# Optimization experiments

Hardware: AMD Instinct MI355X
Metric: run time of the kernel (lower is better)

## Reference

```python
import jax, jax.numpy as jnp
import numpy as np

HEAD_DIM = 64
NUM_HEADS = 16
ROPE_BASE = 10000.0


def _rope_cos_sin(seq_len, head_dim, dtype):
    inv_freq = 1.0 / (ROPE_BASE ** (jnp.arange(0, head_dim, 2, dtype=jnp.float32) / head_dim))
    t = jnp.arange(seq_len, dtype=jnp.float32)
    freqs = jnp.outer(t, inv_freq)                      # [S, D/2]
    emb = jnp.concatenate([freqs, freqs], axis=-1)      # [S, D]
    return jnp.cos(emb).astype(dtype), jnp.sin(emb).astype(dtype)


def _rotate_half(x):
    x1, x2 = jnp.split(x, 2, axis=-1)
    return jnp.concatenate([-x2, x1], axis=-1)


def setup_inputs() -> dict:
    key = jax.random.key(0)
    ks = jax.random.split(key, 5)
    B, S, H = 2, 2048, 1024
    x = jax.random.normal(ks[0], (B, S, H), dtype=jnp.float32)
    attention_mask = jnp.ones((B, S), dtype=jnp.float32)
    scale = 0.02
    Wq = jax.random.normal(ks[1], (H, H), dtype=jnp.float32) * scale
    Wk = jax.random.normal(ks[2], (H, H), dtype=jnp.float32) * scale
    Wv = jax.random.normal(ks[3], (H, H), dtype=jnp.float32) * scale
    Wo = jax.random.normal(ks[4], (H, H), dtype=jnp.float32) * scale
    return {"x": x, "attention_mask": attention_mask, "Wq": Wq, "Wk": Wk, "Wv": Wv, "Wo": Wo}


def reference(x, attention_mask, Wq, Wk, Wv, Wo):
    B, S, H = x.shape
    nh, hd = NUM_HEADS, HEAD_DIM
    scale = hd ** -0.5

    # nn.Linear semantics: y = x @ W^T  (W is [out, in])
    q = jnp.einsum('bsh,oh->bso', x, Wq).reshape(B, S, nh, hd).transpose(0, 2, 1, 3)
    k = jnp.einsum('bsh,oh->bso', x, Wk).reshape(B, S, nh, hd).transpose(0, 2, 1, 3)
    v = jnp.einsum('bsh,oh->bso', x, Wv).reshape(B, S, nh, hd).transpose(0, 2, 1, 3)

    cos, sin = _rope_cos_sin(S, hd, x.dtype)            # [S, hd]
    cos = cos[None, None, :, :]
    sin = sin[None, None, :, :]
    q = q * cos + _rotate_half(q) * sin
    k = k * cos + _rotate_half(k) * sin

    attn = jnp.einsum('bhqd,bhkd->bhqk', q, k) * scale  # [B, nh, S, S]
    mask = (1.0 - attention_mask.astype(x.dtype))[:, None, None, :] * jnp.finfo(x.dtype).min
    attn = attn + mask
    attn = jax.nn.softmax(attn, axis=-1)
    out = jnp.einsum('bhqk,bhkd->bhqd', attn, v)        # [B, nh, S, hd]
    out = out.transpose(0, 2, 1, 3).reshape(B, S, nh * hd)
    return jnp.einsum('bso,ho->bsh', out, Wo)
```

## Files before the change

kernel.cpp:

```cpp
#include <hip/hip_runtime.h>
#include <math.h>

#define BB 2
#define SS 2048
#define HH 1024
#define NH 16
#define HD 64
#define MM (BB*SS)

typedef __attribute__((ext_vector_type(8))) _Float16 f16x8;
typedef __attribute__((ext_vector_type(2))) __fp16 hf16x2;
typedef __attribute__((ext_vector_type(4))) float f32x4;
typedef __attribute__((ext_vector_type(16))) float f32x16;

#define QSCALE 0.18033688011112042f

__device__ __forceinline__ unsigned short f2h(float f) {
    union { _Float16 h; unsigned short u; } c;
    c.h = (_Float16)f;
    return c.u;
}

__device__ __forceinline__ unsigned int pkh(float a, float b) {
    union { hf16x2 h; unsigned int u; } c;
    c.h = __builtin_amdgcn_cvt_pkrtz(a, b);
    return c.u;
}

__device__ __forceinline__ void gld16(const void* g, void* s) {
    __builtin_amdgcn_global_load_lds(
        (const __attribute__((address_space(1))) void*)g,
        (__attribute__((address_space(3))) void*)s, 16, 0, 0);
}

__global__ __launch_bounds__(256) void prep(
    const float* __restrict__ x, const float* __restrict__ mask,
    const float* __restrict__ Wq, const float* __restrict__ Wk,
    const float* __restrict__ Wv, const float* __restrict__ Wo,
    unsigned short* __restrict__ xf, unsigned short* __restrict__ wf,
    float* __restrict__ ctab, float* __restrict__ stab, float* __restrict__ mt,
    unsigned int* __restrict__ mflag)
{
    int gtid = blockIdx.x * 256 + threadIdx.x;
    if (gtid < SS * 32) {
        int s = gtid >> 5, i = gtid & 31;
        double invf = pow(10000.0, -(double)i / 32.0);
        double a = (double)s * invf;
        ctab[gtid] = (float)cos(a);
        stab[gtid] = (float)sin(a);
    }
    if (gtid < BB * SS) {
        float mv = mask[gtid];
        mt[gtid] = (1.0f - mv) * (-1.0e38f);
        unsigned long long bal = __ballot(mv == 1.0f);
        if ((threadIdx.x & 63) == 0)
            mflag[gtid >> 6] = (bal == ~0ull) ? 1u : 0u;
    }
    for (int it = gtid; it < 2097152; it += 524288) {
        float4 v; unsigned short* d; size_t off;
        if (it < 1048576) {
            off = (size_t)it * 4;
            v = *(const float4*)(x + off);
            d = xf;
        } else {
            off = (size_t)(it - 1048576) * 4;
            int row = (int)(off >> 10);
            const float* W = row < 1024 ? Wq : row < 2048 ? Wk : row < 3072 ? Wv : Wo;
            v = *(const float4*)(W + (((size_t)(row & 1023)) << 10) + (off & 1023));
            d = wf;
        }
        *(ushort4*)(d + off) = make_ushort4(f2h(v.x), f2h(v.y), f2h(v.z), f2h(v.w));
    }
}

template<int MODE>
__global__ __launch_bounds__(256, 3) void gemm3(
    const unsigned short* __restrict__ Axf,
    const unsigned short* __restrict__ Wf,
    const float* __restrict__ ctab, const float* __restrict__ stab,
    unsigned short* __restrict__ qo, unsigned short* __restrict__ ko,
    unsigned short* __restrict__ vo, float* __restrict__ fout)
{
    __shared__ __align__(16) short lsA[2][128*32];
    __shared__ __align__(16) short lsB[2][128*32];

    const int t = threadIdx.x;
    const int m0 = blockIdx.x * 128;
    const int brow0 = (MODE == 0 ? 0 : 3072) + blockIdx.y * 128;
    const int lane = t & 63, wv = t >> 6;
    const int wm = (wv >> 1) * 64, wn = (wv & 1) * 64;
    const int fr = lane & 15, fg = lane >> 4;

    const int srow = t >> 2, pc = t & 3;
    const int scx = (pc ^ ((srow >> 1) & 3)) * 8;
    const int lo  = srow * 32 + pc * 8;
    const size_t gA0 = (size_t)(m0 + srow) * HH + scx;
    const size_t gA1 = (size_t)(m0 + 64 + srow) * HH + scx;
    const size_t gB0 = (size_t)(brow0 + srow) * HH + scx;
    const size_t gB1 = (size_t)(brow0 + 64 + srow) * HH + scx;

    f32x4 acc[4][4] = {};

#define STAGE(sel, kk) do { \
        gld16(Axf + gA0 + (kk), &lsA[sel][lo]);            \
        gld16(Wf  + gB0 + (kk), &lsB[sel][lo]);            \
        gld16(Axf + gA1 + (kk), &lsA[sel][lo + 64*32]);    \
        gld16(Wf  + gB1 + (kk), &lsB[sel][lo + 64*32]);    \
    } while (0)

    STAGE(0, 0);
    __syncthreads();

    int cur = 0;
    for (int k0 = 0; k0 < HH; k0 += 32) {
        if (k0 + 32 < HH) STAGE(cur ^ 1, k0 + 32);

        f16x8 ah[4], bh[4];
        const int swz = (fg ^ ((fr >> 1) & 3)) * 8;
        #pragma unroll
        for (int mi = 0; mi < 4; ++mi)
            ah[mi] = *(const f16x8*)&lsA[cur][(wm + 16*mi + fr)*32 + swz];
        #pragma unroll
        for (int ni = 0; ni < 4; ++ni)
            bh[ni] = *(const f16x8*)&lsB[cur][(wn + 16*ni + fr)*32 + swz];

        __builtin_amdgcn_s_setprio(1);
        #pragma unroll
        for (int mi = 0; mi < 4; ++mi)
            #pragma unroll
            for (int ni = 0; ni < 4; ++ni)
                acc[mi][ni] = __builtin_amdgcn_mfma_f32_16x16x32_f16(ah[mi], bh[ni], acc[mi][ni], 0, 0, 0);
        __builtin_amdgcn_s_setprio(0);
        __syncthreads();
        cur ^= 1;
    }
#undef STAGE

    if (MODE == 0) {
        const int mat = brow0 >> 10;
        const int obase = (brow0 & 1023) + wn;
        const int h = obase >> 6;
        #pragma unroll
        for (int mi = 0; mi < 4; ++mi)
            #pragma unroll
            for (int rr = 0; rr < 4; ++rr) {
                int m = m0 + wm + 16*mi + 4*fg + rr;
                int b = m >> 11, s = m & (SS - 1);
                float v[4];
                #pragma unroll
                for (int ni = 0; ni < 4; ++ni) v[ni] = acc[mi][ni][rr];
                if (mat < 2) {
                    #pragma unroll
                    for (int ni = 0; ni < 2; ++ni) {
                        int i = 16*ni + fr;
                        float c = ctab[s*32 + i], sn = stab[s*32 + i];
                        float v1 = v[ni], v2 = v[ni + 2];
                        v[ni]     = v1*c - v2*sn;
                        v[ni + 2] = v2*c + v1*sn;
                    }
                }
                if (mat == 0) {
                    #pragma unroll
                    for (int ni = 0; ni < 4; ++ni) v[ni] *= QSCALE;
                }
                size_t base = ((size_t)(b*NH + h) * SS + s) * HD;
                #pragma unroll
                for (int ni = 0; ni < 4; ++ni) {
                    int d = 16*ni + fr;
                    unsigned short hb = f2h(v[ni]);
                    if (mat == 0)      qo[base + d] = hb;
                    else if (mat == 1) ko[base + (d ^ ((s & 7) << 3))] = hb;
                    else {
                        size_t va = ((size_t)(b*NH + h) * HD + d) * SS
                                  + (s & ~63) + ((s & 63) ^ ((d & 7) << 3));
                        vo[va] = hb;
                    }
                }
            }
    } else {
        const int n0 = blockIdx.y * 128 + wn;
        #pragma unroll
        for (int mi = 0; mi < 4; ++mi)
            #pragma unroll
            for (int rr = 0; rr < 4; ++rr) {
                int m = m0 + wm + 16*mi + 4*fg + rr;
                #pragma unroll
                for (int ni = 0; ni < 4; ++ni)
                    fout[(size_t)m * HH + n0 + 16*ni + fr] = acc[mi][ni][rr];
            }
    }
}

__global__ __launch_bounds__(256, 2) void attn(
    const unsigned short* __restrict__ qg, const unsigned short* __restrict__ kg,
    const unsigned short* __restrict__ vtg, const float* __restrict__ mt,
    const unsigned int* __restrict__ mfl, unsigned short* __restrict__ cf)
{
    __shared__ __align__(16) short Ks[2][64*64];
    __shared__ __align__(16) short Vs[2][64*64];

    const int t = threadIdx.x, lane = t & 63, wv = t >> 6;
    const int ql = lane & 31;
    const int u  = lane >> 5;
    const int qx = ql & 7;
    const int flat = blockIdx.x;
    const int bh = (flat & 7) + ((flat >> 7) << 3);
    const int q0 = ((flat >> 3) & 15) * 128;
    const int b = bh >> 4, h = bh & 15;

    const unsigned short* kgb = kg  + (size_t)bh*SS*HD;
    const unsigned short* vgb = vtg + (size_t)bh*HD*SS;
    const float* mtb = mt + (size_t)b*SS;
    const unsigned int* mfb = mfl + b*32;

    f16x8 qa[4];
    #pragma unroll
    for (int dc = 0; dc < 4; ++dc)
        qa[dc] = *(const f16x8*)&qg[((size_t)bh*SS + q0 + 32*wv + ql)*HD + 16*dc + 8*u];

    f32x16 o[2] = {};
    float lpart = 0.f;

    const int srow = t >> 3, sg = t & 7;

    gld16(kgb + (size_t)srow*HD + sg*8,      &Ks[0][srow*64 + sg*8]);
    gld16(kgb + (size_t)(32+srow)*HD + sg*8, &Ks[0][(32+srow)*64 + sg*8]);
    gld16(vgb + (size_t)srow*SS + sg*8,      &Vs[0][srow*64 + sg*8]);
    gld16(vgb + (size_t)(32+srow)*SS + sg*8, &Vs[0][(32+srow)*64 + sg*8]);
    __syncthreads();

    int cur = 0;
    for (int kt = 0; kt < SS/64; ++kt) {
        const int k0 = kt * 64;
        if (kt + 1 < SS/64) {
            const int kn = k0 + 64;
            gld16(kgb + (size_t)(kn+srow)*HD + sg*8,      &Ks[cur^1][srow*64 + sg*8]);
            gld16(kgb + (size_t)(kn+32+srow)*HD + sg*8,   &Ks[cur^1][(32+srow)*64 + sg*8]);
            gld16(vgb + (size_t)srow*SS + kn + sg*8,      &Vs[cur^1][srow*64 + sg*8]);
            gld16(vgb + (size_t)(32+srow)*SS + kn + sg*8, &Vs[cur^1][(32+srow)*64 + sg*8]);
        }
        const int fl = __builtin_amdgcn_readfirstlane(mfb[kt]);

        f16x8 kb[2][4];
        #pragma unroll
        for (int ktl = 0; ktl < 2; ++ktl)
            #pragma unroll
            for (int dc = 0; dc < 4; ++dc)
                kb[ktl][dc] = *(const f16x8*)&Ks[cur][(32*ktl + ql)*64 + ((2*dc + u) ^ qx)*8];

        f32x16 sc[2] = {};
        __builtin_amdgcn_s_setprio(1);
        #pragma unroll
        for (int dc = 0; dc < 4; ++dc)
            #pragma unroll
            for (int ktl = 0; ktl < 2; ++ktl)
                sc[ktl] = __builtin_amdgcn_mfma_f32_32x32x16_f16(kb[ktl][dc], qa[dc], sc[ktl], 0, 0, 0);
        __builtin_amdgcn_s_setprio(0);

        f16x8 vb[2][4];
        #pragma unroll
        for (int dt = 0; dt < 2; ++dt)
            #pragma unroll
            for (int ki = 0; ki < 4; ++ki)
                vb[dt][ki] = *(const f16x8*)&Vs[cur][(32*dt + ql)*64 + ((2*ki + u) ^ qx)*8];

        if (fl) {
            #pragma unroll
            for (int ktl = 0; ktl < 2; ++ktl)
                #pragma unroll
                for (int r = 0; r < 16; ++r) {
                    float p = __builtin_amdgcn_exp2f(sc[ktl][r]);
                    sc[ktl][r] = p;
                    lpart += p;
                }
        } else {
            #pragma unroll
            for (int ktl = 0; ktl < 2; ++ktl)
                #pragma unroll
                for (int g = 0; g < 4; ++g) {
                    float4 m4 = *(const float4*)&mtb[k0 + 32*ktl + 8*g + 4*u];
                    #pragma unroll
                    for (int j = 0; j < 4; ++j) {
                        float p = __builtin_amdgcn_exp2f(sc[ktl][4*g + j] + (&m4.x)[j]);
                        sc[ktl][4*g + j] = p;
                        lpart += p;
                    }
                }
        }

        __builtin_amdgcn_s_setprio(1);
        #pragma unroll
        for (int ki = 0; ki < 4; ++ki) {
            const int ktl = ki >> 1;
            const int R0 = 8 * (ki & 1);
            unsigned int A0 = pkh(sc[ktl][R0+0], sc[ktl][R0+1]);
            unsigned int A1 = pkh(sc[ktl][R0+2], sc[ktl][R0+3]);
            unsigned int B0 = pkh(sc[ktl][R0+4], sc[ktl][R0+5]);
            unsigned int B1 = pkh(sc[ktl][R0+6], sc[ktl][R0+7]);
            asm volatile("v_permlane32_swap_b32 %0, %1" : "+v"(A0), "+v"(B0));
            asm volatile("v_permlane32_swap_b32 %0, %1" : "+v"(A1), "+v"(B1));
            union { unsigned int w[4]; f16x8 v; } pf;
            pf.w[0] = A0; pf.w[1] = A1; pf.w[2] = B0; pf.w[3] = B1;
            #pragma unroll
            for (int dt = 0; dt < 2; ++dt)
                o[dt] = __builtin_amdgcn_mfma_f32_32x32x16_f16(vb[dt][ki], pf.v, o[dt], 0, 0, 0);
        }
        __builtin_amdgcn_s_setprio(0);
        __syncthreads();
        cur ^= 1;
    }

    float l = lpart + __shfl_xor(lpart, 32);
    float inv = 1.0f / l;
    size_t base = ((size_t)b*SS + q0 + 32*wv + ql)*HH + h*HD;
    #pragma unroll
    for (int dt = 0; dt < 2; ++dt)
        #pragma unroll
        for (int g = 0; g < 4; ++g) {
            uint2 w;
            w.x = pkh(o[dt][4*g+0]*inv, o[dt][4*g+1]*inv);
            w.y = pkh(o[dt][4*g+2]*inv, o[dt][4*g+3]*inv);
            *(uint2*)&cf[base + 32*dt + 8*g + 4*u] = w;
        }
}

extern "C" void kernel_launch(void* const* d_in, const int* in_sizes, int n_in,
                              void* d_out, int out_size, void* d_ws, size_t ws_size,
                              hipStream_t stream) {
    const float* x    = (const float*)d_in[0];
    const float* mask = (const float*)d_in[1];
    const float* Wq   = (const float*)d_in[2];
    const float* Wk   = (const float*)d_in[3];
    const float* Wv   = (const float*)d_in[4];
    const float* Wo   = (const float*)d_in[5];
    float* out = (float*)d_out;

    const size_t T = (size_t)MM * HH;
    unsigned short* xf = (unsigned short*)d_ws;
    unsigned short* wf = xf + T;
    unsigned short* qt = wf + T;
    unsigned short* kt = qt + T;
    unsigned short* vt = kt + T;
    float* ctab = (float*)(vt + T);
    float* stab = ctab + SS*32;
    float* mt   = stab + SS*32;
    unsigned int* mfg = (unsigned int*)(mt + BB*SS);
    unsigned short* cf = xf;

    prep<<<2048, 256, 0, stream>>>(x, mask, Wq, Wk, Wv, Wo, xf, wf, ctab, stab, mt, mfg);
    gemm3<0><<<dim3(MM/128, 3*HH/128), 256, 0, stream>>>(xf, wf, ctab, stab,
                                                         qt, kt, vt, nullptr);
    attn<<<512, 256, 0, stream>>>(qt, kt, vt, mt, mfg, cf);
    gemm3<1><<<dim3(MM/128, HH/128), 256, 0, stream>>>(cf, wf, nullptr, nullptr,
                                                       nullptr, nullptr, nullptr, out);
}
```

Baseline: 114.5 us.

## Split attention key tiles across waves and reduce partial outputs through LDS

Each attention block now covers 64 queries instead of 128, and its four waves form a 2x2 split: two query halves times two key halves of every 64-key tile. The grid doubles to 1024 blocks, and launch bounds go from 2 to 4 blocks per CU to fit the smaller per-wave register state. At the end, the partial row sums and output accumulators from the second key-half waves are combined through shared memory. This trades more K/V tile loads per query and an extra LDS reduction with barriers for higher occupancy and more blocks to spread across the GPU.

```diff
diff --git a/kernel.cpp b/kernel.cpp
--- a/kernel.cpp
+++ b/kernel.cpp
@@ -191,7 +191,7 @@
     }
 }
 
-__global__ __launch_bounds__(256, 2) void attn(
+__global__ __launch_bounds__(256, 4) void attn(
     const unsigned short* __restrict__ qg, const unsigned short* __restrict__ kg,
     const unsigned short* __restrict__ vtg, const float* __restrict__ mt,
     const unsigned int* __restrict__ mfl, unsigned short* __restrict__ cf)
@@ -203,9 +203,10 @@
     const int ql = lane & 31;
     const int u  = lane >> 5;
     const int qx = ql & 7;
+    const int qh = wv & 1, kh = wv >> 1;
     const int flat = blockIdx.x;
-    const int bh = (flat & 7) + ((flat >> 7) << 3);
-    const int q0 = ((flat >> 3) & 15) * 128;
+    const int bh = (flat & 7) + ((flat >> 8) << 3);
+    const int q0 = ((flat >> 3) & 31) * 64;
     const int b = bh >> 4, h = bh & 15;
 
     const unsigned short* kgb = kg  + (size_t)bh*SS*HD;
@@ -216,7 +217,7 @@
     f16x8 qa[4];
     #pragma unroll
     for (int dc = 0; dc < 4; ++dc)
-        qa[dc] = *(const f16x8*)&qg[((size_t)bh*SS + q0 + 32*wv + ql)*HD + 16*dc + 8*u];
+        qa[dc] = *(const f16x8*)&qg[((size_t)bh*SS + q0 + 32*qh + ql)*HD + 16*dc + 8*u];
 
     f32x16 o[2] = {};
     float lpart = 0.f;
@@ -241,62 +242,53 @@
         }
         const int fl = __builtin_amdgcn_readfirstlane(mfb[kt]);
 
-        f16x8 kb[2][4];
-        #pragma unroll
-        for (int ktl = 0; ktl < 2; ++ktl)
-            #pragma unroll
-            for (int dc = 0; dc < 4; ++dc)
-                kb[ktl][dc] = *(const f16x8*)&Ks[cur][(32*ktl + ql)*64 + ((2*dc + u) ^ qx)*8];
-
-        f32x16 sc[2] = {};
+        f16x8 kb[4];
+        #pragma unroll
+        for (int dc = 0; dc < 4; ++dc)
+            kb[dc] = *(const f16x8*)&Ks[cur][(32*kh + ql)*64 + ((2*dc + u) ^ qx)*8];
+
+        f32x16 sc = {};
         __builtin_amdgcn_s_setprio(1);
         #pragma unroll
         for (int dc = 0; dc < 4; ++dc)
-            #pragma unroll
-            for (int ktl = 0; ktl < 2; ++ktl)
-                sc[ktl] = __builtin_amdgcn_mfma_f32_32x32x16_f16(kb[ktl][dc], qa[dc], sc[ktl], 0, 0, 0);
+            sc = __builtin_amdgcn_mfma_f32_32x32x16_f16(kb[dc], qa[dc], sc, 0, 0, 0);
         __builtin_amdgcn_s_setprio(0);
 
-        f16x8 vb[2][4];
+        f16x8 vb[2][2];
         #pragma unroll
         for (int dt = 0; dt < 2; ++dt)
             #pragma unroll
-            for (int ki = 0; ki < 4; ++ki)
-                vb[dt][ki] = *(const f16x8*)&Vs[cur][(32*dt + ql)*64 + ((2*ki + u) ^ qx)*8];
+            for (int ki = 0; ki < 2; ++ki)
+                vb[dt][ki] = *(const f16x8*)&Vs[cur][(32*dt + ql)*64 + ((4*kh + 2*ki + u) ^ qx)*8];
 
         if (fl) {
             #pragma unroll
-            for (int ktl = 0; ktl < 2; ++ktl)
+            for (int r = 0; r < 16; ++r) {
+                float p = __builtin_amdgcn_exp2f(sc[r]);
+                sc[r] = p;
+                lpart += p;
+            }
+        } else {
+            #pragma unroll
+            for (int g = 0; g < 4; ++g) {
+                float4 m4 = *(const float4*)&mtb[k0 + 32*kh + 8*g + 4*u];
                 #pragma unroll
-                for (int r = 0; r < 16; ++r) {
-                    float p = __builtin_amdgcn_exp2f(sc[ktl][r]);
-                    sc[ktl][r] = p;
+                for (int j = 0; j < 4; ++j) {
+                    float p = __builtin_amdgcn_exp2f(sc[4*g + j] + (&m4.x)[j]);
+                    sc[4*g + j] = p;
                     lpart += p;
                 }
-        } else {
-            #pragma unroll
-            for (int ktl = 0; ktl < 2; ++ktl)
-                #pragma unroll
-                for (int g = 0; g < 4; ++g) {
-                    float4 m4 = *(const float4*)&mtb[k0 + 32*ktl + 8*g + 4*u];
-                    #pragma unroll
-                    for (int j = 0; j < 4; ++j) {
-                        float p = __builtin_amdgcn_exp2f(sc[ktl][4*g + j] + (&m4.x)[j]);
-                        sc[ktl][4*g + j] = p;
-                        lpart += p;
-                    }
-                }
+            }
         }
 
         __builtin_amdgcn_s_setprio(1);
         #pragma unroll
-        for (int ki = 0; ki < 4; ++ki) {
-            const int ktl = ki >> 1;
-            const int R0 = 8 * (ki & 1);
-            unsigned int A0 = pkh(sc[ktl][R0+0], sc[ktl][R0+1]);
-            unsigned int A1 = pkh(sc[ktl][R0+2], sc[ktl][R0+3]);
-            unsigned int B0 = pkh(sc[ktl][R0+4], sc[ktl][R0+5]);
-            unsigned int B1 = pkh(sc[ktl][R0+6], sc[ktl][R0+7]);
+        for (int ki = 0; ki < 2; ++ki) {
+            const int R0 = 8 * ki;
+            unsigned int A0 = pkh(sc[R0+0], sc[R0+1]);
+            unsigned int A1 = pkh(sc[R0+2], sc[R0+3]);
+            unsigned int B0 = pkh(sc[R0+4], sc[R0+5]);
+            unsigned int B1 = pkh(sc[R0+6], sc[R0+7]);
             asm volatile("v_permlane32_swap_b32 %0, %1" : "+v"(A0), "+v"(B0));
             asm volatile("v_permlane32_swap_b32 %0, %1" : "+v"(A1), "+v"(B1));
             union { unsigned int w[4]; f16x8 v; } pf;
@@ -310,18 +302,38 @@
         cur ^= 1;
     }
 
-    float l = lpart + __shfl_xor(lpart, 32);
-    float inv = 1.0f / l;
-    size_t base = ((size_t)b*SS + q0 + 32*wv + ql)*HH + h*HD;
+    float* lscr = (float*)Vs;
+    float* oscr = (float*)Ks;
+    if (kh == 1) lscr[qh*64 + lane] = lpart;
+    __syncthreads();
+    float inv = 0.f;
+    if (kh == 0) {
+        float l = lpart + lscr[qh*64 + lane];
+        l += __shfl_xor(l, 32);
+        inv = 1.0f / l;
+    }
+    const size_t base = ((size_t)b*SS + q0 + 32*qh + ql)*HH + h*HD;
     #pragma unroll
-    for (int dt = 0; dt < 2; ++dt)
-        #pragma unroll
-        for (int g = 0; g < 4; ++g) {
-            uint2 w;
-            w.x = pkh(o[dt][4*g+0]*inv, o[dt][4*g+1]*inv);
-            w.y = pkh(o[dt][4*g+2]*inv, o[dt][4*g+3]*inv);
-            *(uint2*)&cf[base + 32*dt + 8*g + 4*u] = w;
-        }
+    for (int dt = 0; dt < 2; ++dt) {
+        __syncthreads();
+        if (kh == 1) {
+            #pragma unroll
+            for (int r = 0; r < 16; ++r)
+                oscr[r*128 + qh*64 + lane] = o[dt][r];
+        }
+        __syncthreads();
+        if (kh == 0) {
+            #pragma unroll
+            for (int g = 0; g < 4; ++g) {
+                float v0 = (o[dt][4*g+0] + oscr[(4*g+0)*128 + qh*64 + lane]) * inv;
+                float v1 = (o[dt][4*g+1] + oscr[(4*g+1)*128 + qh*64 + lane]) * inv;
+                float v2 = (o[dt][4*g+2] + oscr[(4*g+2)*128 + qh*64 + lane]) * inv;
+                float v3 = (o[dt][4*g+3] + oscr[(4*g+3)*128 + qh*64 + lane]) * inv;
+                uint2 w; w.x = pkh(v0, v1); w.y = pkh(v2, v3);
+                *(uint2*)&cf[base + 32*dt + 8*g + 4*u] = w;
+            }
+        }
+    }
 }
 
 extern "C" void kernel_launch(void* const* d_in, const int* in_sizes, int n_in,
@@ -350,7 +362,7 @@
     prep<<<2048, 256, 0, stream>>>(x, mask, Wq, Wk, Wv, Wo, xf, wf, ctab, stab, mt, mfg);
     gemm3<0><<<dim3(MM/128, 3*HH/128), 256, 0, stream>>>(xf, wf, ctab, stab,
                                                          qt, kt, vt, nullptr);
-    attn<<<512, 256, 0, stream>>>(qt, kt, vt, mt, mfg, cf);
+    attn<<<1024, 256, 0, stream>>>(qt, kt, vt, mt, mfg, cf);
     gemm3<1><<<dim3(MM/128, HH/128), 256, 0, stream>>>(cf, wf, nullptr, nullptr,
                                                        nullptr, nullptr, nullptr, out);
 }
```

After: 117.1 us. 1.02x slower.
